# Optimization experiments

Hardware: AMD Instinct MI355X
Metric: run time of the kernel (lower is better)

The kernel has to match this reference:

```python
import jax, jax.numpy as jnp
import numpy as np

EPS = 1e-5


def sage_conv(x, src, dst, Wl, Wr, b, n):
    # PyG SAGEConv: out_i = W_l * mean_{j in N(i)} x_j + W_r * x_i + b
    agg = jax.ops.segment_sum(x[src], dst, num_segments=n)  # [N, d]
    deg = jax.ops.segment_sum(jnp.ones_like(src, dtype=x.dtype), dst, num_segments=n)
    agg = agg / jnp.maximum(deg, 1.0)[:, None]
    return agg @ Wl + x @ Wr + b


def setup_inputs() -> dict:
    key = jax.random.key(0)
    ks = jax.random.split(key, 12)
    N, E, D_IN, D_H, D_OUT = 50000, 600000, 128, 128, 64
    x = jax.random.normal(ks[0], (N, D_IN), dtype=jnp.float32)
    edge_index = jax.random.randint(ks[1], (2, E), 0, N, dtype=jnp.int64)
    s_in = 1.0 / np.sqrt(D_IN)
    s_h = 1.0 / np.sqrt(D_H)
    return {
        "x": x,
        "edge_index": edge_index,
        "Wl0": jax.random.normal(ks[2], (D_IN, D_H), jnp.float32) * s_in,
        "Wr0": jax.random.normal(ks[3], (D_IN, D_H), jnp.float32) * s_in,
        "b0": jnp.zeros((D_H,), jnp.float32),
        "Wl1": jax.random.normal(ks[4], (D_H, D_H), jnp.float32) * s_h,
        "Wr1": jax.random.normal(ks[5], (D_H, D_H), jnp.float32) * s_h,
        "b1": jnp.zeros((D_H,), jnp.float32),
        "Wl2": jax.random.normal(ks[6], (D_H, D_OUT), jnp.float32) * s_h,
        "Wr2": jax.random.normal(ks[7], (D_H, D_OUT), jnp.float32) * s_h,
        "b2": jnp.zeros((D_OUT,), jnp.float32),
        "gamma": jnp.ones((D_H,), jnp.float32),
        "beta": jnp.zeros((D_H,), jnp.float32),
    }


def reference(x, edge_index, Wl0, Wr0, b0, Wl1, Wr1, b1, Wl2, Wr2, b2, gamma, beta):
    n = x.shape[0]
    src, dst = edge_index[0], edge_index[1]
    residual = x  # in_channels == hidden_channels -> no residual_transform
    # layer 0: conv + relu (+ dropout as identity in eval)
    h = jax.nn.relu(sage_conv(x, src, dst, Wl0, Wr0, b0, n))
    # middle layer: conv + BN(batch stats) + relu + residual
    h = sage_conv(h, src, dst, Wl1, Wr1, b1, n)
    mu = jnp.mean(h, axis=0)
    var = jnp.var(h, axis=0)  # biased, as in torch BN normalization
    h = (h - mu) * jax.lax.rsqrt(var + EPS) * gamma + beta
    h = jax.nn.relu(h) + residual
    # output layer
    h = sage_conv(h, src, dst, Wl2, Wr2, b2, n)
    return jax.nn.log_softmax(h, axis=-1)
```

## Files before the change

kernel.cpp:

```cpp
#include <hip/hip_runtime.h>
#include <hip/hip_bf16.h>


#define WS_EPS 1e-5f

typedef unsigned short ushort_t;
typedef unsigned int uint_t;
typedef ushort_t ushort8 __attribute__((ext_vector_type(8)));
typedef short short8 __attribute__((ext_vector_type(8)));
typedef float f32x4 __attribute__((ext_vector_type(4)));

__device__ __forceinline__ float bf2f(ushort_t u) {
    return __uint_as_float(((uint_t)u) << 16);
}
__device__ __forceinline__ ushort_t f2bf(float f) {
    uint_t u = __float_as_uint(f);
    u = (u + 0x7fffu + ((u >> 16) & 1u)) >> 16;
    return (ushort_t)u;
}

__global__ __launch_bounds__(256) void k_deg(const int* __restrict__ ei,
                                             int* __restrict__ deg, int E) {
    int e = blockIdx.x * 256 + threadIdx.x;
    if (e < E) atomicAdd(&deg[ei[E + e]], 1);
}

constexpr int SCHUNK = 4096;

__global__ __launch_bounds__(256) void k_scan_part(const int* __restrict__ deg,
                                                   int* __restrict__ bsum, int n) {
    int t = threadIdx.x;
    int base = blockIdx.x * SCHUNK + t * 16;
    int s = 0;
#pragma unroll
    for (int j = 0; j < 16; ++j) {
        int i = base + j;
        if (i < n) s += deg[i];
    }
#pragma unroll
    for (int d = 1; d < 64; d <<= 1) s += __shfl_xor(s, d);
    __shared__ int wt[4];
    if ((t & 63) == 0) wt[t >> 6] = s;
    __syncthreads();
    if (t == 0) bsum[blockIdx.x] = wt[0] + wt[1] + wt[2] + wt[3];
}

__global__ __launch_bounds__(64) void k_scan_bsum(const int* __restrict__ bsum,
                                                  int* __restrict__ boff,
                                                  int* __restrict__ off_n, int nb) {
    int lane = threadIdx.x;
    int carry = 0;
    for (int base = 0; base < nb; base += 64) {
        int t = base + lane;
        int v = (t < nb) ? bsum[t] : 0;
        int x = v;
#pragma unroll
        for (int d = 1; d < 64; d <<= 1) {
            int y = __shfl_up(x, d);
            if (lane >= d) x += y;
        }
        if (t < nb) boff[t] = carry + x - v;
        carry += __shfl(x, 63);
    }
    if (lane == 0) *off_n = carry;
}

__global__ __launch_bounds__(256) void k_scan_apply(const int* __restrict__ deg,
                                                    const int* __restrict__ boff,
                                                    int* __restrict__ off, int n) {
    int t = threadIdx.x;
    int lane = t & 63, wid = t >> 6;
    int base = blockIdx.x * SCHUNK + t * 16;
    int v[16];
    int s = 0;
#pragma unroll
    for (int j = 0; j < 16; ++j) {
        int i = base + j;
        v[j] = (i < n) ? deg[i] : 0;
        s += v[j];
    }
    int x = s;
#pragma unroll
    for (int d = 1; d < 64; d <<= 1) {
        int y = __shfl_up(x, d);
        if (lane >= d) x += y;
    }
    __shared__ int wtot[4];
    if (lane == 63) wtot[wid] = x;
    __syncthreads();
    int woff = 0;
    for (int wj = 0; wj < wid; ++wj) woff += wtot[wj];
    int run = boff[blockIdx.x] + woff + x - s;
#pragma unroll
    for (int j = 0; j < 16; ++j) {
        int i = base + j;
        if (i < n) off[i] = run;
        run += v[j];
    }
}

__global__ __launch_bounds__(256) void k_scatter(const int* __restrict__ ei,
                                                 const int* __restrict__ off,
                                                 int* __restrict__ cur,
                                                 int* __restrict__ csr, int E) {
    int e = blockIdx.x * 256 + threadIdx.x;
    if (e < E) {
        int d = ei[E + e];
        int s = ei[e];
        int p = atomicAdd(&cur[d], 1);
        csr[off[d] + p] = s;
    }
}

__global__ __launch_bounds__(256) void k_prep(const float* __restrict__ x,
                                              ushort_t* __restrict__ xb, int total2,
                                              int nb_cvt,
                                              const float* __restrict__ Wl0,
                                              const float* __restrict__ Wr0,
                                              const float* __restrict__ Wl1,
                                              const float* __restrict__ Wr1,
                                              const float* __restrict__ Wl2,
                                              const float* __restrict__ Wr2,
                                              ushort_t* __restrict__ wts) {
    int b = blockIdx.x;
    if (b < nb_cvt) {
        int i = b * 256 + threadIdx.x;
        if (i >= total2) return;
        float2 v = *(const float2*)&x[(size_t)i * 2];
        uint_t p = (uint_t)f2bf(v.x) | ((uint_t)f2bf(v.y) << 16);
        *(uint_t*)&xb[(size_t)i * 2] = p;
        return;
    }
    int id = (b - nb_cvt) * 256 + threadIdx.x;
    if (id >= 81920) return;
    const float* W;
    int rel, nout, base;
    if (id < 65536) {
        int m = id >> 14;
        rel = id & 16383;
        nout = 128;
        base = m << 14;
        W = (m == 0) ? Wl0 : (m == 1) ? Wr0 : (m == 2) ? Wl1 : Wr1;
    } else {
        int m = (id - 65536) >> 13;
        rel = (id - 65536) & 8191;
        nout = 64;
        base = 65536 + (m << 13);
        W = (m == 0) ? Wl2 : Wr2;
    }
    int c = rel >> 7;
    int k = rel & 127;
    wts[base + rel] = f2bf(W[(size_t)k * nout + c]);
}

template <int EPI>
__global__ __launch_bounds__(256, 4) void k_fgemm(const ushort_t* __restrict__ X1,
                                                  const ushort_t* __restrict__ W1,
                                                  const ushort_t* __restrict__ X2,
                                                  const ushort_t* __restrict__ W2,
                                                  const float* __restrict__ bias,
                                                  void* __restrict__ outv,
                                                  float* __restrict__ stats, int n) {
    constexpr int NOUT = 128, K = 128, BM = 64, LDK = 136;
    constexpr int FM = 2, FN = 4;

    __shared__ ushort_t Xs[2][BM * LDK];
    __shared__ float sred[256];

    const int t = threadIdx.x;
    const int row0 = blockIdx.x * BM;
    const int lane = t & 63;
    const int wid = t >> 6;
    const int wr = wid >> 1, wc = wid & 1;
    const int r16 = lane & 15, kb = lane >> 4;
    const int tr = t >> 4, seg = t & 15;

    if (EPI == 1) sred[t] = 0.f;

    ushort8 g[4];
#pragma unroll
    for (int u = 0; u < 4; ++u) {
        int gr = row0 + u * 16 + tr;
        g[u] = (gr < n) ? *(const ushort8*)&X1[(size_t)gr * K + seg * 8] : (ushort8)0;
    }
#pragma unroll
    for (int u = 0; u < 4; ++u)
        *(ushort8*)&Xs[0][(u * 16 + tr) * LDK + seg * 8] = g[u];
    __syncthreads();

#pragma unroll
    for (int u = 0; u < 4; ++u) {
        int gr = row0 + u * 16 + tr;
        g[u] = (gr < n) ? *(const ushort8*)&X2[(size_t)gr * K + seg * 8] : (ushort8)0;
    }

    f32x4 acc[FM][FN];
#pragma unroll
    for (int i = 0; i < FM; ++i)
#pragma unroll
        for (int j = 0; j < FN; ++j) acc[i][j] = (f32x4)0.f;

#pragma unroll
    for (int ks = 0; ks < 4; ++ks) {
        short8 a[FM], b[FN];
#pragma unroll
        for (int fm = 0; fm < FM; ++fm)
            a[fm] = *(const short8*)&Xs[0][(wr * 32 + fm * 16 + r16) * LDK + ks * 32 + kb * 8];
#pragma unroll
        for (int fn = 0; fn < FN; ++fn)
            b[fn] = *(const short8*)&W1[(size_t)(wc * 64 + fn * 16 + r16) * K + ks * 32 + kb * 8];
#pragma unroll
        for (int fm = 0; fm < FM; ++fm)
#pragma unroll
            for (int fn = 0; fn < FN; ++fn)
                acc[fm][fn] = __builtin_amdgcn_mfma_f32_16x16x32_bf16(a[fm], b[fn], acc[fm][fn], 0, 0, 0);
    }

#pragma unroll
    for (int u = 0; u < 4; ++u)
        *(ushort8*)&Xs[1][(u * 16 + tr) * LDK + seg * 8] = g[u];
    __syncthreads();

#pragma unroll
    for (int ks = 0; ks < 4; ++ks) {
        short8 a[FM], b[FN];
#pragma unroll
        for (int fm = 0; fm < FM; ++fm)
            a[fm] = *(const short8*)&Xs[1][(wr * 32 + fm * 16 + r16) * LDK + ks * 32 + kb * 8];
#pragma unroll
        for (int fn = 0; fn < FN; ++fn)
            b[fn] = *(const short8*)&W2[(size_t)(wc * 64 + fn * 16 + r16) * K + ks * 32 + kb * 8];
#pragma unroll
        for (int fm = 0; fm < FM; ++fm)
#pragma unroll
            for (int fn = 0; fn < FN; ++fn)
                acc[fm][fn] = __builtin_amdgcn_mfma_f32_16x16x32_bf16(a[fm], b[fn], acc[fm][fn], 0, 0, 0);
    }

    if constexpr (EPI == 2) {
#pragma unroll
        for (int fm = 0; fm < FM; ++fm) {
#pragma unroll
            for (int r = 0; r < 4; ++r) {
                int row = row0 + wr * 32 + fm * 16 + kb * 4 + r;
                if (row >= n) continue;
#pragma unroll
                for (int fn = 0; fn < FN; ++fn) {
                    int col = wc * 64 + fn * 16 + r16;
                    float v = acc[fm][fn][r] + bias[col];
                    ((ushort_t*)outv)[(size_t)row * NOUT + col] = f2bf(fmaxf(v, 0.f));
                }
            }
        }
    } else {
        float s[FN], q[FN];
#pragma unroll
        for (int fn = 0; fn < FN; ++fn) { s[fn] = 0.f; q[fn] = 0.f; }
#pragma unroll
        for (int fm = 0; fm < FM; ++fm) {
#pragma unroll
            for (int r = 0; r < 4; ++r) {
                int row = row0 + wr * 32 + fm * 16 + kb * 4 + r;
                if (row >= n) continue;
#pragma unroll
                for (int fn = 0; fn < FN; ++fn) {
                    int col = wc * 64 + fn * 16 + r16;
                    float v = acc[fm][fn][r] + bias[col];
                    ((float*)outv)[(size_t)row * NOUT + col] = v;
                    s[fn] += v;
                    q[fn] += v * v;
                }
            }
        }
#pragma unroll
        for (int fn = 0; fn < FN; ++fn) {
            s[fn] += __shfl_xor(s[fn], 16);
            s[fn] += __shfl_xor(s[fn], 32);
            q[fn] += __shfl_xor(q[fn], 16);
            q[fn] += __shfl_xor(q[fn], 32);
        }
        if (kb == 0) {
#pragma unroll
            for (int fn = 0; fn < FN; ++fn) {
                int col = wc * 64 + fn * 16 + r16;
                atomicAdd(&sred[col], s[fn]);
                atomicAdd(&sred[128 + col], q[fn]);
            }
        }
        __syncthreads();
        atomicAdd(&stats[t], sred[t]);
    }
}

template <int EPI>
__global__ __launch_bounds__(256, 4) void k_mgemm64(const ushort_t* __restrict__ X,
                                                    const ushort_t* __restrict__ WT,
                                                    const ushort_t* __restrict__ AGG,
                                                    const float* __restrict__ bias,
                                                    void* __restrict__ outv, int n) {
    constexpr int NOUT = 64, K = 128, BM = 64, LDK = 136;
    constexpr int FN = 4;

    __shared__ ushort_t Xs[BM * LDK];

    const int t = threadIdx.x;
    const int row0 = blockIdx.x * BM;
    const int lane = t & 63;
    const int wid = t >> 6;
    const int r16 = lane & 15, kb = lane >> 4;
    const int tr = t >> 4, seg = t & 15;

#pragma unroll
    for (int u = 0; u < 4; ++u) {
        int gr = row0 + u * 16 + tr;
        ushort8 v = (gr < n) ? *(const ushort8*)&X[(size_t)gr * K + seg * 8] : (ushort8)0;
        *(ushort8*)&Xs[(u * 16 + tr) * LDK + seg * 8] = v;
    }
    __syncthreads();

    f32x4 acc[FN];
#pragma unroll
    for (int j = 0; j < FN; ++j) acc[j] = (f32x4)0.f;

#pragma unroll
    for (int ks = 0; ks < 4; ++ks) {
        short8 a = *(const short8*)&Xs[(wid * 16 + r16) * LDK + ks * 32 + kb * 8];
        short8 b[FN];
#pragma unroll
        for (int fn = 0; fn < FN; ++fn)
            b[fn] = *(const short8*)&WT[(size_t)(fn * 16 + r16) * K + ks * 32 + kb * 8];
#pragma unroll
        for (int fn = 0; fn < FN; ++fn)
            acc[fn] = __builtin_amdgcn_mfma_f32_16x16x32_bf16(a, b[fn], acc[fn], 0, 0, 0);
    }

    if constexpr (EPI == 3) {
        float* outp = (float*)outv;
#pragma unroll
        for (int r = 0; r < 4; ++r) {
            int row = row0 + wid * 16 + kb * 4 + r;
            bool ok = (row < n);
            float vv[FN];
#pragma unroll
            for (int fn = 0; fn < FN; ++fn) {
                int col = fn * 16 + r16;
                vv[fn] = ok ? (acc[fn][r] + bf2f(AGG[(size_t)row * NOUT + col]) + bias[col])
                            : 0.f;
            }
            float m = fmaxf(fmaxf(vv[0], vv[1]), fmaxf(vv[2], vv[3]));
#pragma unroll
            for (int d = 1; d < 16; d <<= 1) m = fmaxf(m, __shfl_xor(m, d));
            float e = expf(vv[0] - m) + expf(vv[1] - m) + expf(vv[2] - m) + expf(vv[3] - m);
#pragma unroll
            for (int d = 1; d < 16; d <<= 1) e += __shfl_xor(e, d);
            float lg = m + logf(e);
            if (ok) {
#pragma unroll
                for (int fn = 0; fn < FN; ++fn)
                    outp[(size_t)row * NOUT + fn * 16 + r16] = vv[fn] - lg;
            }
        }
    } else {
#pragma unroll
        for (int r = 0; r < 4; ++r) {
            int row = row0 + wid * 16 + kb * 4 + r;
            if (row >= n) continue;
#pragma unroll
            for (int fn = 0; fn < FN; ++fn) {
                int col = fn * 16 + r16;
                ((ushort_t*)outv)[(size_t)row * NOUT + col] = f2bf(acc[fn][r]);
            }
        }
    }
}

template <int D>
__global__ __launch_bounds__(256) void k_segmean_bf(const ushort_t* __restrict__ U,
                                                    const int* __restrict__ off,
                                                    const int* __restrict__ srcs,
                                                    ushort_t* __restrict__ out,
                                                    int n) {
    int node = blockIdx.x * 8 + (threadIdx.x >> 5);
    int sub = threadIdx.x & 31;
    if (node >= n) return;
    int beg = off[node], end = off[node + 1];
    constexpr int CPL = D / 32;
    float a0 = 0.f, a1 = 0.f, a2 = 0.f, a3 = 0.f;
    int i = beg;
    for (; i + 8 <= end; i += 8) {
        int sv[8];
#pragma unroll
        for (int u = 0; u < 8; ++u) sv[u] = srcs[i + u];
#pragma unroll
        for (int u = 0; u < 8; ++u) {
            if (CPL == 4) {
                uint2 v = *(const uint2*)&U[(size_t)sv[u] * D + sub * 4];
                a0 += __uint_as_float(v.x << 16);
                a1 += __uint_as_float(v.x & 0xffff0000u);
                a2 += __uint_as_float(v.y << 16);
                a3 += __uint_as_float(v.y & 0xffff0000u);
            } else {
                uint_t v = *(const uint_t*)&U[(size_t)sv[u] * D + sub * 2];
                a0 += __uint_as_float(v << 16);
                a1 += __uint_as_float(v & 0xffff0000u);
            }
        }
    }
    for (; i + 4 <= end; i += 4) {
        int sv[4];
#pragma unroll
        for (int u = 0; u < 4; ++u) sv[u] = srcs[i + u];
#pragma unroll
        for (int u = 0; u < 4; ++u) {
            if (CPL == 4) {
                uint2 v = *(const uint2*)&U[(size_t)sv[u] * D + sub * 4];
                a0 += __uint_as_float(v.x << 16);
                a1 += __uint_as_float(v.x & 0xffff0000u);
                a2 += __uint_as_float(v.y << 16);
                a3 += __uint_as_float(v.y & 0xffff0000u);
            } else {
                uint_t v = *(const uint_t*)&U[(size_t)sv[u] * D + sub * 2];
                a0 += __uint_as_float(v << 16);
                a1 += __uint_as_float(v & 0xffff0000u);
            }
        }
    }
    for (; i < end; ++i) {
        int s = srcs[i];
        if (CPL == 4) {
            uint2 v = *(const uint2*)&U[(size_t)s * D + sub * 4];
            a0 += __uint_as_float(v.x << 16);
            a1 += __uint_as_float(v.x & 0xffff0000u);
            a2 += __uint_as_float(v.y << 16);
            a3 += __uint_as_float(v.y & 0xffff0000u);
        } else {
            uint_t v = *(const uint_t*)&U[(size_t)s * D + sub * 2];
            a0 += __uint_as_float(v << 16);
            a1 += __uint_as_float(v & 0xffff0000u);
        }
    }
    int d = end - beg;
    float inv = 1.f / (float)(d > 1 ? d : 1);
    if (CPL == 4) {
        uint2 p;
        p.x = (uint_t)f2bf(a0 * inv) | ((uint_t)f2bf(a1 * inv) << 16);
        p.y = (uint_t)f2bf(a2 * inv) | ((uint_t)f2bf(a3 * inv) << 16);
        *(uint2*)&out[(size_t)node * D + sub * 4] = p;
    } else {
        uint_t p = (uint_t)f2bf(a0 * inv) | ((uint_t)f2bf(a1 * inv) << 16);
        *(uint_t*)&out[(size_t)node * D + sub * 2] = p;
    }
}

__global__ __launch_bounds__(256) void k_bnapply(const float* __restrict__ P,
                                                 const float* __restrict__ X,
                                                 const float* __restrict__ stats,
                                                 const float* __restrict__ gamma,
                                                 const float* __restrict__ beta,
                                                 ushort_t* __restrict__ H, int n) {
    int i = blockIdx.x * 256 + threadIdx.x;
    if (i >= n * 64) return;
    int nd = i >> 6;
    int c = (i & 63) << 1;
    float inv_n = 1.f / (float)n;
    float mu0 = stats[c] * inv_n, mu1 = stats[c + 1] * inv_n;
    float v0 = stats[128 + c] * inv_n - mu0 * mu0;
    float v1 = stats[128 + c + 1] * inv_n - mu1 * mu1;
    float s0 = rsqrtf(v0 + WS_EPS) * gamma[c];
    float s1 = rsqrtf(v1 + WS_EPS) * gamma[c + 1];
    float2 p = *(const float2*)&P[(size_t)nd * 128 + c];
    float2 xr = *(const float2*)&X[(size_t)nd * 128 + c];
    float h0 = fmaxf((p.x - mu0) * s0 + beta[c], 0.f) + xr.x;
    float h1 = fmaxf((p.y - mu1) * s1 + beta[c + 1], 0.f) + xr.y;
    uint_t pk = (uint_t)f2bf(h0) | ((uint_t)f2bf(h1) << 16);
    *(uint_t*)&H[(size_t)nd * 128 + c] = pk;
}

extern "C" void kernel_launch(void* const* d_in, const int* in_sizes, int n_in,
                              void* d_out, int out_size, void* d_ws, size_t ws_size,
                              hipStream_t stream) {
    const float* x     = (const float*)d_in[0];
    const int*   ei    = (const int*)d_in[1];
    const float* Wl0   = (const float*)d_in[2];
    const float* Wr0   = (const float*)d_in[3];
    const float* b0    = (const float*)d_in[4];
    const float* Wl1   = (const float*)d_in[5];
    const float* Wr1   = (const float*)d_in[6];
    const float* b1    = (const float*)d_in[7];
    const float* Wl2   = (const float*)d_in[8];
    const float* Wr2   = (const float*)d_in[9];
    const float* b2    = (const float*)d_in[10];
    const float* gamma = (const float*)d_in[11];
    const float* beta  = (const float*)d_in[12];

    const int n = in_sizes[0] / 128;
    const int E = in_sizes[1] / 2;
    const int nb_scan = (n + SCHUNK - 1) / SCHUNK;

    char* w = (char*)d_ws;
    auto alloc = [&](size_t bytes) -> void* {
        void* p = (void*)w;
        w += (bytes + 255) & ~(size_t)255;
        return p;
    };
    int*      deg   = (int*)alloc((size_t)n * 4);
    int*      cur   = (int*)alloc((size_t)n * 4);
    float*    stats = (float*)alloc(256 * 4);
    size_t    zbytes = (size_t)((char*)w - (char*)deg);
    int*      off   = (int*)alloc(((size_t)n + 1) * 4);
    int*      csr   = (int*)alloc((size_t)E * 4);
    int*      bsum  = (int*)alloc(256 * 4);
    int*      boff  = (int*)alloc(256 * 4);
    ushort_t* wts   = (ushort_t*)alloc((size_t)81920 * 2);
    ushort_t* xb    = (ushort_t*)alloc((size_t)n * 128 * 2);
    ushort_t* H     = (ushort_t*)alloc((size_t)n * 128 * 2);
    float*    P     = (float*)alloc((size_t)n * 128 * 4);
    ushort_t* slabB = (ushort_t*)alloc((size_t)n * 128 * 2);

    ushort_t* WtL0 = wts;
    ushort_t* WtR0 = wts + 16384;
    ushort_t* WtL1 = wts + 32768;
    ushort_t* WtR1 = wts + 49152;
    ushort_t* WtL2 = wts + 65536;
    ushort_t* WtR2 = wts + 73728;

    ushort_t* M   = slabB;
    ushort_t* A64 = slabB;
    ushort_t* B64 = slabB + (size_t)n * 64;

    hipMemsetAsync(deg, 0, zbytes, stream);

    const int eb = (E + 255) / 256;
    k_deg<<<eb, 256, 0, stream>>>(ei, deg, E);
    k_scan_part<<<nb_scan, 256, 0, stream>>>(deg, bsum, n);
    k_scan_bsum<<<1, 64, 0, stream>>>(bsum, boff, off + n, nb_scan);
    k_scan_apply<<<nb_scan, 256, 0, stream>>>(deg, boff, off, n);
    k_scatter<<<eb, 256, 0, stream>>>(ei, off, cur, csr, E);

    const int nb_cvt = (n * 64 + 255) / 256;
    k_prep<<<nb_cvt + 320, 256, 0, stream>>>(x, xb, n * 64, nb_cvt,
                                             Wl0, Wr0, Wl1, Wr1, Wl2, Wr2, wts);

    const int gb = (n + 63) / 64;
    const int smb = (n + 7) / 8;

    k_segmean_bf<128><<<smb, 256, 0, stream>>>(xb, off, csr, M, n);
    k_fgemm<2><<<gb, 256, 0, stream>>>(xb, WtR0, M, WtL0, b0, H, nullptr, n);

    k_segmean_bf<128><<<smb, 256, 0, stream>>>(H, off, csr, M, n);
    k_fgemm<1><<<gb, 256, 0, stream>>>(H, WtR1, M, WtL1, b1, P, stats, n);
    k_bnapply<<<(n * 64 + 255) / 256, 256, 0, stream>>>(P, x, stats, gamma, beta, H, n);

    k_mgemm64<0><<<gb, 256, 0, stream>>>(H, WtL2, nullptr, nullptr, A64, n);
    k_segmean_bf<64><<<smb, 256, 0, stream>>>(A64, off, csr, B64, n);
    k_mgemm64<3><<<gb, 256, 0, stream>>>(H, WtR2, B64, b2, (float*)d_out, n);
}
```

Measured before the change: 255.6 us.

## Replace LDS-staged GEMMs with register-direct per-wave GEMMs, bf16 BN intermediate, wider gathers

Merges the two GEMM kernels into one templated kernel where each wave loads its 16-row A fragments straight from global memory into registers, with no LDS staging or barriers. The pre-BatchNorm intermediate is stored in bf16 instead of fp32, halving its write and read traffic, at some cost in precision. The segment-mean gather now has each lane load 8 bf16 values (16 bytes) per neighbour row. The GEMM launch bound drops to 2 blocks per SM, and weight fragments are re-read from global/L2 by every wave.

```diff
diff --git a/kernel.cpp b/kernel.cpp
--- a/kernel.cpp
+++ b/kernel.cpp
@@ -153,123 +153,88 @@
     wts[base + rel] = f2bf(W[(size_t)k * nout + c]);
 }
 
-template <int EPI>
-__global__ __launch_bounds__(256, 4) void k_fgemm(const ushort_t* __restrict__ X1,
+template <int NOUT, int EPI>
+__global__ __launch_bounds__(256, 2) void k_rgemm(const ushort_t* __restrict__ X1,
                                                   const ushort_t* __restrict__ W1,
                                                   const ushort_t* __restrict__ X2,
                                                   const ushort_t* __restrict__ W2,
+                                                  const ushort_t* __restrict__ AGG,
                                                   const float* __restrict__ bias,
                                                   void* __restrict__ outv,
                                                   float* __restrict__ stats, int n) {
-    constexpr int NOUT = 128, K = 128, BM = 64, LDK = 136;
-    constexpr int FM = 2, FN = 4;
-
-    __shared__ ushort_t Xs[2][BM * LDK];
-    __shared__ float sred[256];
+    constexpr int K = 128;
+    constexpr int FN = NOUT / 16;
+    constexpr bool DUAL = (EPI == 1 || EPI == 2);
 
     const int t = threadIdx.x;
-    const int row0 = blockIdx.x * BM;
     const int lane = t & 63;
-    const int wid = t >> 6;
-    const int wr = wid >> 1, wc = wid & 1;
     const int r16 = lane & 15, kb = lane >> 4;
-    const int tr = t >> 4, seg = t & 15;
-
-    if (EPI == 1) sred[t] = 0.f;
-
-    ushort8 g[4];
-#pragma unroll
-    for (int u = 0; u < 4; ++u) {
-        int gr = row0 + u * 16 + tr;
-        g[u] = (gr < n) ? *(const ushort8*)&X1[(size_t)gr * K + seg * 8] : (ushort8)0;
-    }
-#pragma unroll
-    for (int u = 0; u < 4; ++u)
-        *(ushort8*)&Xs[0][(u * 16 + tr) * LDK + seg * 8] = g[u];
-    __syncthreads();
-
-#pragma unroll
-    for (int u = 0; u < 4; ++u) {
-        int gr = row0 + u * 16 + tr;
-        g[u] = (gr < n) ? *(const ushort8*)&X2[(size_t)gr * K + seg * 8] : (ushort8)0;
-    }
-
-    f32x4 acc[FM][FN];
-#pragma unroll
-    for (int i = 0; i < FM; ++i)
-#pragma unroll
-        for (int j = 0; j < FN; ++j) acc[i][j] = (f32x4)0.f;
-
-#pragma unroll
-    for (int ks = 0; ks < 4; ++ks) {
-        short8 a[FM], b[FN];
-#pragma unroll
-        for (int fm = 0; fm < FM; ++fm)
-            a[fm] = *(const short8*)&Xs[0][(wr * 32 + fm * 16 + r16) * LDK + ks * 32 + kb * 8];
-#pragma unroll
-        for (int fn = 0; fn < FN; ++fn)
-            b[fn] = *(const short8*)&W1[(size_t)(wc * 64 + fn * 16 + r16) * K + ks * 32 + kb * 8];
-#pragma unroll
-        for (int fm = 0; fm < FM; ++fm)
-#pragma unroll
-            for (int fn = 0; fn < FN; ++fn)
-                acc[fm][fn] = __builtin_amdgcn_mfma_f32_16x16x32_bf16(a[fm], b[fn], acc[fm][fn], 0, 0, 0);
-    }
-
-#pragma unroll
-    for (int u = 0; u < 4; ++u)
-        *(ushort8*)&Xs[1][(u * 16 + tr) * LDK + seg * 8] = g[u];
-    __syncthreads();
-
-#pragma unroll
-    for (int ks = 0; ks < 4; ++ks) {
-        short8 a[FM], b[FN];
-#pragma unroll
-        for (int fm = 0; fm < FM; ++fm)
-            a[fm] = *(const short8*)&Xs[1][(wr * 32 + fm * 16 + r16) * LDK + ks * 32 + kb * 8];
-#pragma unroll
-        for (int fn = 0; fn < FN; ++fn)
-            b[fn] = *(const short8*)&W2[(size_t)(wc * 64 + fn * 16 + r16) * K + ks * 32 + kb * 8];
-#pragma unroll
-        for (int fm = 0; fm < FM; ++fm)
-#pragma unroll
-            for (int fn = 0; fn < FN; ++fn)
-                acc[fm][fn] = __builtin_amdgcn_mfma_f32_16x16x32_bf16(a[fm], b[fn], acc[fm][fn], 0, 0, 0);
+    const int wv = blockIdx.x * 4 + (t >> 6);
+    const int base = wv * 16;
+    const int arow = base + r16;
+    const bool rok = (arow < n);
+    const size_t xoff = (size_t)arow * K + kb * 8;
+
+    f32x4 acc[FN];
+#pragma unroll
+    for (int j = 0; j < FN; ++j) acc[j] = (f32x4)0.f;
+
+    {
+        short8 a[4];
+#pragma unroll
+        for (int ks = 0; ks < 4; ++ks)
+            a[ks] = rok ? *(const short8*)&X1[xoff + ks * 32] : (short8)0;
+#pragma unroll
+        for (int ks = 0; ks < 4; ++ks) {
+#pragma unroll
+            for (int fn = 0; fn < FN; ++fn) {
+                short8 b = *(const short8*)&W1[(size_t)(fn * 16 + r16) * K + ks * 32 + kb * 8];
+                acc[fn] = __builtin_amdgcn_mfma_f32_16x16x32_bf16(a[ks], b, acc[fn], 0, 0, 0);
+            }
+        }
+    }
+    if constexpr (DUAL) {
+        short8 a[4];
+#pragma unroll
+        for (int ks = 0; ks < 4; ++ks)
+            a[ks] = rok ? *(const short8*)&X2[xoff + ks * 32] : (short8)0;
+#pragma unroll
+        for (int ks = 0; ks < 4; ++ks) {
+#pragma unroll
+            for (int fn = 0; fn < FN; ++fn) {
+                short8 b = *(const short8*)&W2[(size_t)(fn * 16 + r16) * K + ks * 32 + kb * 8];
+                acc[fn] = __builtin_amdgcn_mfma_f32_16x16x32_bf16(a[ks], b, acc[fn], 0, 0, 0);
+            }
+        }
     }
 
     if constexpr (EPI == 2) {
 #pragma unroll
-        for (int fm = 0; fm < FM; ++fm) {
-#pragma unroll
-            for (int r = 0; r < 4; ++r) {
-                int row = row0 + wr * 32 + fm * 16 + kb * 4 + r;
-                if (row >= n) continue;
-#pragma unroll
-                for (int fn = 0; fn < FN; ++fn) {
-                    int col = wc * 64 + fn * 16 + r16;
-                    float v = acc[fm][fn][r] + bias[col];
-                    ((ushort_t*)outv)[(size_t)row * NOUT + col] = f2bf(fmaxf(v, 0.f));
-                }
-            }
-        }
-    } else {
+        for (int r = 0; r < 4; ++r) {
+            int row = base + kb * 4 + r;
+            if (row >= n) continue;
+#pragma unroll
+            for (int fn = 0; fn < FN; ++fn) {
+                int col = fn * 16 + r16;
+                float v = acc[fn][r] + bias[col];
+                ((ushort_t*)outv)[(size_t)row * NOUT + col] = f2bf(fmaxf(v, 0.f));
+            }
+        }
+    } else if constexpr (EPI == 1) {
         float s[FN], q[FN];
 #pragma unroll
         for (int fn = 0; fn < FN; ++fn) { s[fn] = 0.f; q[fn] = 0.f; }
 #pragma unroll
-        for (int fm = 0; fm < FM; ++fm) {
-#pragma unroll
-            for (int r = 0; r < 4; ++r) {
-                int row = row0 + wr * 32 + fm * 16 + kb * 4 + r;
-                if (row >= n) continue;
-#pragma unroll
-                for (int fn = 0; fn < FN; ++fn) {
-                    int col = wc * 64 + fn * 16 + r16;
-                    float v = acc[fm][fn][r] + bias[col];
-                    ((float*)outv)[(size_t)row * NOUT + col] = v;
-                    s[fn] += v;
-                    q[fn] += v * v;
-                }
+        for (int r = 0; r < 4; ++r) {
+            int row = base + kb * 4 + r;
+            if (row >= n) continue;
+#pragma unroll
+            for (int fn = 0; fn < FN; ++fn) {
+                int col = fn * 16 + r16;
+                float v = acc[fn][r] + bias[col];
+                ((ushort_t*)outv)[(size_t)row * NOUT + col] = f2bf(v);
+                s[fn] += v;
+                q[fn] += v * v;
             }
         }
 #pragma unroll
@@ -279,66 +244,35 @@
             q[fn] += __shfl_xor(q[fn], 16);
             q[fn] += __shfl_xor(q[fn], 32);
         }
+        __shared__ float sred[256];
+        sred[t] = 0.f;
+        __syncthreads();
         if (kb == 0) {
 #pragma unroll
             for (int fn = 0; fn < FN; ++fn) {
-                int col = wc * 64 + fn * 16 + r16;
+                int col = fn * 16 + r16;
                 atomicAdd(&sred[col], s[fn]);
                 atomicAdd(&sred[128 + col], q[fn]);
             }
         }
         __syncthreads();
         atomicAdd(&stats[t], sred[t]);
-    }
-}
-
-template <int EPI>
-__global__ __launch_bounds__(256, 4) void k_mgemm64(const ushort_t* __restrict__ X,
-                                                    const ushort_t* __restrict__ WT,
-                                                    const ushort_t* __restrict__ AGG,
-                                                    const float* __restrict__ bias,
-                                                    void* __restrict__ outv, int n) {
-    constexpr int NOUT = 64, K = 128, BM = 64, LDK = 136;
-    constexpr int FN = 4;
-
-    __shared__ ushort_t Xs[BM * LDK];
-
-    const int t = threadIdx.x;
-    const int row0 = blockIdx.x * BM;
-    const int lane = t & 63;
-    const int wid = t >> 6;
-    const int r16 = lane & 15, kb = lane >> 4;
-    const int tr = t >> 4, seg = t & 15;
-
-#pragma unroll
-    for (int u = 0; u < 4; ++u) {
-        int gr = row0 + u * 16 + tr;
-        ushort8 v = (gr < n) ? *(const ushort8*)&X[(size_t)gr * K + seg * 8] : (ushort8)0;
-        *(ushort8*)&Xs[(u * 16 + tr) * LDK + seg * 8] = v;
-    }
-    __syncthreads();
-
-    f32x4 acc[FN];
-#pragma unroll
-    for (int j = 0; j < FN; ++j) acc[j] = (f32x4)0.f;
-
-#pragma unroll
-    for (int ks = 0; ks < 4; ++ks) {
-        short8 a = *(const short8*)&Xs[(wid * 16 + r16) * LDK + ks * 32 + kb * 8];
-        short8 b[FN];
-#pragma unroll
-        for (int fn = 0; fn < FN; ++fn)
-            b[fn] = *(const short8*)&WT[(size_t)(fn * 16 + r16) * K + ks * 32 + kb * 8];
-#pragma unroll
-        for (int fn = 0; fn < FN; ++fn)
-            acc[fn] = __builtin_amdgcn_mfma_f32_16x16x32_bf16(a, b[fn], acc[fn], 0, 0, 0);
-    }
-
-    if constexpr (EPI == 3) {
+    } else if constexpr (EPI == 0) {
+#pragma unroll
+        for (int r = 0; r < 4; ++r) {
+            int row = base + kb * 4 + r;
+            if (row >= n) continue;
+#pragma unroll
+            for (int fn = 0; fn < FN; ++fn) {
+                int col = fn * 16 + r16;
+                ((ushort_t*)outv)[(size_t)row * NOUT + col] = f2bf(acc[fn][r]);
+            }
+        }
+    } else {
         float* outp = (float*)outv;
 #pragma unroll
         for (int r = 0; r < 4; ++r) {
-            int row = row0 + wid * 16 + kb * 4 + r;
+            int row = base + kb * 4 + r;
             bool ok = (row < n);
             float vv[FN];
 #pragma unroll
@@ -358,17 +292,6 @@
 #pragma unroll
                 for (int fn = 0; fn < FN; ++fn)
                     outp[(size_t)row * NOUT + fn * 16 + r16] = vv[fn] - lg;
-            }
-        }
-    } else {
-#pragma unroll
-        for (int r = 0; r < 4; ++r) {
-            int row = row0 + wid * 16 + kb * 4 + r;
-            if (row >= n) continue;
-#pragma unroll
-            for (int fn = 0; fn < FN; ++fn) {
-                int col = fn * 16 + r16;
-                ((ushort_t*)outv)[(size_t)row * NOUT + col] = f2bf(acc[fn][r]);
             }
         }
     }
@@ -380,12 +303,15 @@
                                                     const int* __restrict__ srcs,
                                                     ushort_t* __restrict__ out,
                                                     int n) {
-    int node = blockIdx.x * 8 + (threadIdx.x >> 5);
-    int sub = threadIdx.x & 31;
+    constexpr int L = D / 8;
+    constexpr int PER = 256 / L;
+    int node = blockIdx.x * PER + threadIdx.x / L;
+    int sub = threadIdx.x % L;
     if (node >= n) return;
     int beg = off[node], end = off[node + 1];
-    constexpr int CPL = D / 32;
-    float a0 = 0.f, a1 = 0.f, a2 = 0.f, a3 = 0.f;
+    float a[8];
+#pragma unroll
+    for (int j = 0; j < 8; ++j) a[j] = 0.f;
     int i = beg;
     for (; i + 8 <= end; i += 8) {
         int sv[8];
@@ -393,17 +319,9 @@
         for (int u = 0; u < 8; ++u) sv[u] = srcs[i + u];
 #pragma unroll
         for (int u = 0; u < 8; ++u) {
-            if (CPL == 4) {
-                uint2 v = *(const uint2*)&U[(size_t)sv[u] * D + sub * 4];
-                a0 += __uint_as_float(v.x << 16);
-                a1 += __uint_as_float(v.x & 0xffff0000u);
-                a2 += __uint_as_float(v.y << 16);
-                a3 += __uint_as_float(v.y & 0xffff0000u);
-            } else {
-                uint_t v = *(const uint_t*)&U[(size_t)sv[u] * D + sub * 2];
-                a0 += __uint_as_float(v << 16);
-                a1 += __uint_as_float(v & 0xffff0000u);
-            }
+            ushort8 v = *(const ushort8*)&U[(size_t)sv[u] * D + sub * 8];
+#pragma unroll
+            for (int j = 0; j < 8; ++j) a[j] += bf2f((ushort_t)v[j]);
         }
     }
     for (; i + 4 <= end; i += 4) {
@@ -412,47 +330,25 @@
         for (int u = 0; u < 4; ++u) sv[u] = srcs[i + u];
 #pragma unroll
         for (int u = 0; u < 4; ++u) {
-            if (CPL == 4) {
-                uint2 v = *(const uint2*)&U[(size_t)sv[u] * D + sub * 4];
-                a0 += __uint_as_float(v.x << 16);
-                a1 += __uint_as_float(v.x & 0xffff0000u);
-                a2 += __uint_as_float(v.y << 16);
-                a3 += __uint_as_float(v.y & 0xffff0000u);
-            } else {
-                uint_t v = *(const uint_t*)&U[(size_t)sv[u] * D + sub * 2];
-                a0 += __uint_as_float(v << 16);
-                a1 += __uint_as_float(v & 0xffff0000u);
-            }
+            ushort8 v = *(const ushort8*)&U[(size_t)sv[u] * D + sub * 8];
+#pragma unroll
+            for (int j = 0; j < 8; ++j) a[j] += bf2f((ushort_t)v[j]);
         }
     }
     for (; i < end; ++i) {
-        int s = srcs[i];
-        if (CPL == 4) {
-            uint2 v = *(const uint2*)&U[(size_t)s * D + sub * 4];
-            a0 += __uint_as_float(v.x << 16);
-            a1 += __uint_as_float(v.x & 0xffff0000u);
-            a2 += __uint_as_float(v.y << 16);
-            a3 += __uint_as_float(v.y & 0xffff0000u);
-        } else {
-            uint_t v = *(const uint_t*)&U[(size_t)s * D + sub * 2];
-            a0 += __uint_as_float(v << 16);
-            a1 += __uint_as_float(v & 0xffff0000u);
-        }
+        ushort8 v = *(const ushort8*)&U[(size_t)srcs[i] * D + sub * 8];
+#pragma unroll
+        for (int j = 0; j < 8; ++j) a[j] += bf2f((ushort_t)v[j]);
     }
     int d = end - beg;
     float inv = 1.f / (float)(d > 1 ? d : 1);
-    if (CPL == 4) {
-        uint2 p;
-        p.x = (uint_t)f2bf(a0 * inv) | ((uint_t)f2bf(a1 * inv) << 16);
-        p.y = (uint_t)f2bf(a2 * inv) | ((uint_t)f2bf(a3 * inv) << 16);
-        *(uint2*)&out[(size_t)node * D + sub * 4] = p;
-    } else {
-        uint_t p = (uint_t)f2bf(a0 * inv) | ((uint_t)f2bf(a1 * inv) << 16);
-        *(uint_t*)&out[(size_t)node * D + sub * 2] = p;
-    }
-}
-
-__global__ __launch_bounds__(256) void k_bnapply(const float* __restrict__ P,
+    ushort8 o;
+#pragma unroll
+    for (int j = 0; j < 8; ++j) o[j] = f2bf(a[j] * inv);
+    *(ushort8*)&out[(size_t)node * D + sub * 8] = o;
+}
+
+__global__ __launch_bounds__(256) void k_bnapply(const ushort_t* __restrict__ P,
                                                  const float* __restrict__ X,
                                                  const float* __restrict__ stats,
                                                  const float* __restrict__ gamma,
@@ -468,10 +364,12 @@
     float v1 = stats[128 + c + 1] * inv_n - mu1 * mu1;
     float s0 = rsqrtf(v0 + WS_EPS) * gamma[c];
     float s1 = rsqrtf(v1 + WS_EPS) * gamma[c + 1];
-    float2 p = *(const float2*)&P[(size_t)nd * 128 + c];
+    uint_t pv = *(const uint_t*)&P[(size_t)nd * 128 + c];
+    float p0 = __uint_as_float(pv << 16);
+    float p1 = __uint_as_float(pv & 0xffff0000u);
     float2 xr = *(const float2*)&X[(size_t)nd * 128 + c];
-    float h0 = fmaxf((p.x - mu0) * s0 + beta[c], 0.f) + xr.x;
-    float h1 = fmaxf((p.y - mu1) * s1 + beta[c + 1], 0.f) + xr.y;
+    float h0 = fmaxf((p0 - mu0) * s0 + beta[c], 0.f) + xr.x;
+    float h1 = fmaxf((p1 - mu1) * s1 + beta[c + 1], 0.f) + xr.y;
     uint_t pk = (uint_t)f2bf(h0) | ((uint_t)f2bf(h1) << 16);
     *(uint_t*)&H[(size_t)nd * 128 + c] = pk;
 }
@@ -514,7 +412,7 @@
     ushort_t* wts   = (ushort_t*)alloc((size_t)81920 * 2);
     ushort_t* xb    = (ushort_t*)alloc((size_t)n * 128 * 2);
     ushort_t* H     = (ushort_t*)alloc((size_t)n * 128 * 2);
-    float*    P     = (float*)alloc((size_t)n * 128 * 4);
+    ushort_t* Pb    = (ushort_t*)alloc((size_t)n * 128 * 2);
     ushort_t* slabB = (ushort_t*)alloc((size_t)n * 128 * 2);
 
     ushort_t* WtL0 = wts;
@@ -541,17 +439,18 @@
     k_prep<<<nb_cvt + 320, 256, 0, stream>>>(x, xb, n * 64, nb_cvt,
                                              Wl0, Wr0, Wl1, Wr1, Wl2, Wr2, wts);
 
-    const int gb = (n + 63) / 64;
-    const int smb = (n + 7) / 8;
-
-    k_segmean_bf<128><<<smb, 256, 0, stream>>>(xb, off, csr, M, n);
-    k_fgemm<2><<<gb, 256, 0, stream>>>(xb, WtR0, M, WtL0, b0, H, nullptr, n);
-
-    k_segmean_bf<128><<<smb, 256, 0, stream>>>(H, off, csr, M, n);
-    k_fgemm<1><<<gb, 256, 0, stream>>>(H, WtR1, M, WtL1, b1, P, stats, n);
-    k_bnapply<<<(n * 64 + 255) / 256, 256, 0, stream>>>(P, x, stats, gamma, beta, H, n);
-
-    k_mgemm64<0><<<gb, 256, 0, stream>>>(H, WtL2, nullptr, nullptr, A64, n);
-    k_segmean_bf<64><<<smb, 256, 0, stream>>>(A64, off, csr, B64, n);
-    k_mgemm64<3><<<gb, 256, 0, stream>>>(H, WtR2, B64, b2, (float*)d_out, n);
-}
+    const int gb = (n / 16 + 3) / 4;
+    const int smb128 = (n + 15) / 16;
+    const int smb64 = (n + 31) / 32;
+
+    k_segmean_bf<128><<<smb128, 256, 0, stream>>>(xb, off, csr, M, n);
+    k_rgemm<128, 2><<<gb, 256, 0, stream>>>(xb, WtR0, M, WtL0, nullptr, b0, H, nullptr, n);
+
+    k_segmean_bf<128><<<smb128, 256, 0, stream>>>(H, off, csr, M, n);
+    k_rgemm<128, 1><<<gb, 256, 0, stream>>>(H, WtR1, M, WtL1, nullptr, b1, Pb, stats, n);
+    k_bnapply<<<(n * 64 + 255) / 256, 256, 0, stream>>>(Pb, x, stats, gamma, beta, H, n);
+
+    k_rgemm<64, 0><<<gb, 256, 0, stream>>>(H, WtL2, nullptr, nullptr, nullptr, nullptr, A64, nullptr, n);
+    k_segmean_bf<64><<<smb64, 256, 0, stream>>>(A64, off, csr, B64, n);
+    k_rgemm<64, 3><<<gb, 256, 0, stream>>>(H, WtR2, nullptr, nullptr, B64, b2, (float*)d_out, nullptr, n);
+}
```

Measured after the change: 282.3 us. 10.4% more time.
